# Optimization experiments

Measured on AMD Instinct MI355X. Metric: run time of the kernel, lower is better.

## Reference

```python
import jax, jax.numpy as jnp
import numpy as np

B, S, I = 64, 64, 512      # batch, seq_len, input_size (encoder hidden)
C = 512                    # context_size (attention dim)
H = 1024                   # decoder hidden (must equal 2*deep_out_size per source)
D = 512                    # deep_out_size
KY = 32000                 # target vocab
M = 512                    # target embedding dim (Ey rows)


def setup_inputs() -> dict:
    key = jax.random.key(0)
    ks = jax.random.split(key, 16)
    sc = 0.05  # small init to keep tanh/softmax in sane range
    return {
        "input_seq": jax.random.normal(ks[0], (B, S, I), jnp.float32),
        "Ey_t": jax.random.normal(ks[1], (KY, M), jnp.float32) * sc,   # Ey.transpose(0,1)
        "W":  jax.random.normal(ks[2], (H, C), jnp.float32) * sc,
        "U":  jax.random.normal(ks[3], (I, C), jnp.float32) * sc,
        "b":  jax.random.normal(ks[4], (C,), jnp.float32) * sc,
        "v":  jax.random.normal(ks[5], (C,), jnp.float32) * sc,
        "W_ih": jax.random.normal(ks[6], (3 * H, C), jnp.float32) * sc,
        "W_hh": jax.random.normal(ks[7], (3 * H, H), jnp.float32) * sc,
        "b_ih": jax.random.normal(ks[8], (3 * H,), jnp.float32) * sc,
        "b_hh": jax.random.normal(ks[9], (3 * H,), jnp.float32) * sc,
        "U_o": jax.random.normal(ks[10], (H, H), jnp.float32) * sc,   # (2*D, hidden) with H==2*D
        "V_o": jax.random.normal(ks[11], (M, H), jnp.float32) * sc,
        "C_o": jax.random.normal(ks[12], (I, H), jnp.float32) * sc,
        "W_o": jax.random.normal(ks[13], (D, KY), jnp.float32) * sc,
    }


def reference(input_seq, Ey_t, W, U, b, v, W_ih, W_hh, b_ih, b_hh, U_o, V_o, C_o, W_o):
    Bn, Sn, In = input_seq.shape
    Hn = W.shape[0]
    Ky = W_o.shape[1]

    # Precompute U_h once, as in source: (B, S, C)
    U_h = jnp.einsum('bsi,ic->bsc', input_seq, U)

    def gru_cell(x, h):
        # torch.nn.GRUCell semantics, gate order r, z, n
        gi = x @ W_ih.T + b_ih
        gh = h @ W_hh.T + b_hh
        i_r, i_z, i_n = jnp.split(gi, 3, axis=-1)
        h_r, h_z, h_n = jnp.split(gh, 3, axis=-1)
        r = jax.nn.sigmoid(i_r + h_r)
        z = jax.nn.sigmoid(i_z + h_z)
        n = jnp.tanh(i_n + r * h_n)
        return (1.0 - z) * n + z * h

    def step(carry, _):
        s, y = carry
        # Additive (Bahdanau) attention over full encoder sequence
        W_s = s @ W                                       # (B, C)
        e = jnp.tanh(W_s[:, None, :] + U_h + b) @ v       # (B, S)
        alpha = jax.nn.softmax(e, axis=1)                 # softmax over seq dim
        ctx = jnp.einsum('bsi,bs->bi', input_seq, alpha)  # (B, I)
        s_new = gru_cell(ctx, s)                          # (B, H)
        # Deep-output with maxout (pool_size=2)
        t = s_new @ U_o + (y @ Ey_t) @ V_o + ctx @ C_o    # (B, 2*D)
        t = t.reshape(Bn, -1, 2).max(axis=-1)             # (B, D)
        prob = jax.nn.softmax(t @ W_o, axis=-1)           # (B, Ky)
        return (s_new, prob), prob

    s0 = jnp.zeros((Bn, Hn), input_seq.dtype)
    y0 = jnp.zeros((Bn, Ky), input_seq.dtype)
    _, probs = jax.lax.scan(step, (s0, y0), None, length=Sn)
    return probs  # (S, B, Ky)
```

## Files before the change

kernel.cpp:

```cpp
#include <hip/hip_runtime.h>
#include <cstdint>
#include <cstddef>

typedef __bf16 bf16;
typedef __bf16 bf16x8 __attribute__((ext_vector_type(8)));
typedef float f32x4 __attribute__((ext_vector_type(4)));

#define MFMA16(a, b, c) __builtin_amdgcn_mfma_f32_16x16x32_bf16((a), (b), (c), 0, 0, 0)

__device__ __forceinline__ float fast_tanh(float x) {
  x = fminf(fmaxf(x, -15.f), 15.f);
  float e = __expf(2.f * x);
  return (e - 1.f) / (e + 1.f);
}
__device__ __forceinline__ float fast_sigmoid(float x) {
  return 1.f / (1.f + __expf(-x));
}


__global__ void cast_split_kernel(const float* __restrict__ src,
                                  bf16* __restrict__ hi, bf16* __restrict__ lo, int n) {
  int i = blockIdx.x * 256 + threadIdx.x;
  if (i < n) {
    float x = src[i];
    bf16 h = (bf16)x;
    hi[i] = h;
    lo[i] = (bf16)(x - (float)h);
  }
}

__global__ void tc_kernel(const float* __restrict__ src, bf16* __restrict__ hi,
                          bf16* __restrict__ lo, int R, int C) {
  __shared__ float tile[32][33];
  int c0 = blockIdx.x * 32, r0 = blockIdx.y * 32;
  int tx = threadIdx.x & 31, ty = threadIdx.x >> 5;
  for (int i = ty; i < 32; i += 8)
    tile[i][tx] = src[(size_t)(r0 + i) * C + c0 + tx];
  __syncthreads();
  for (int i = ty; i < 32; i += 8) {
    float x = tile[tx][i];
    bf16 h = (bf16)x;
    size_t idx = (size_t)(c0 + i) * R + r0 + tx;
    hi[idx] = h;
    if (lo) lo[idx] = (bf16)(x - (float)h);
  }
}


template <int ATOMIC>
__device__ __forceinline__ void gemm_body(const bf16* __restrict__ A, int lda,
                                          const bf16* __restrict__ BT, int ldb,
                                          float* __restrict__ C, int ldc,
                                          int mb, int nb, int k0, int kSteps) {
  int lane = threadIdx.x & 63, wave = threadIdx.x >> 6;
  int mrow = mb * 64 + wave * 16 + (lane & 15);
  int qk = (lane >> 4) * 8;
  const bf16* ap = A + (size_t)mrow * lda + k0 + qk;
  int ncol = nb * 64 + (lane & 15);
  const bf16* bp[4];
#pragma unroll
  for (int j = 0; j < 4; ++j) bp[j] = BT + (size_t)(ncol + 16 * j) * ldb + k0 + qk;
  f32x4 acc[4];
#pragma unroll
  for (int j = 0; j < 4; ++j) acc[j] = {0.f, 0.f, 0.f, 0.f};
  for (int s = 0; s < kSteps; ++s) {
    bf16x8 a = *(const bf16x8*)ap; ap += 32;
#pragma unroll
    for (int j = 0; j < 4; ++j) {
      bf16x8 b = *(const bf16x8*)bp[j]; bp[j] += 32;
      acc[j] = MFMA16(a, b, acc[j]);
    }
  }
  int row = mb * 64 + wave * 16 + (lane >> 4) * 4;
  int col = nb * 64 + (lane & 15);
#pragma unroll
  for (int j = 0; j < 4; ++j)
#pragma unroll
    for (int i = 0; i < 4; ++i) {
      size_t idx = (size_t)(row + i) * ldc + col + j * 16;
      if (ATOMIC) atomicAdd(&C[idx], acc[j][i]); else C[idx] = acc[j][i];
    }
}

__device__ __forceinline__ void gemm_split_body(const bf16* __restrict__ Ahi,
                                                const bf16* __restrict__ Alo, int lda,
                                                const bf16* __restrict__ Bhi,
                                                const bf16* __restrict__ Blo, int ldb,
                                                float* __restrict__ C, int ldc,
                                                int mb, int nb, int kSteps) {
  int lane = threadIdx.x & 63, wave = threadIdx.x >> 6;
  int mrow = mb * 64 + wave * 16 + (lane & 15);
  int qk = (lane >> 4) * 8;
  const bf16* ah = Ahi + (size_t)mrow * lda + qk;
  const bf16* al = Alo + (size_t)mrow * lda + qk;
  int ncol = nb * 64 + (lane & 15);
  const bf16* bh[4]; const bf16* bl[4];
#pragma unroll
  for (int j = 0; j < 4; ++j) {
    bh[j] = Bhi + (size_t)(ncol + 16 * j) * ldb + qk;
    bl[j] = Blo + (size_t)(ncol + 16 * j) * ldb + qk;
  }
  f32x4 acc[4];
#pragma unroll
  for (int j = 0; j < 4; ++j) acc[j] = {0.f, 0.f, 0.f, 0.f};
  for (int s = 0; s < kSteps; ++s) {
    bf16x8 Ah = *(const bf16x8*)ah; ah += 32;
    bf16x8 Al = *(const bf16x8*)al; al += 32;
#pragma unroll
    for (int j = 0; j < 4; ++j) {
      bf16x8 Bh = *(const bf16x8*)bh[j]; bh[j] += 32;
      bf16x8 Bl = *(const bf16x8*)bl[j]; bl[j] += 32;
      acc[j] = MFMA16(Ah, Bh, acc[j]);
      acc[j] = MFMA16(Ah, Bl, acc[j]);
      acc[j] = MFMA16(Al, Bh, acc[j]);
    }
  }
  int row = mb * 64 + wave * 16 + (lane >> 4) * 4;
  int col = nb * 64 + (lane & 15);
#pragma unroll
  for (int j = 0; j < 4; ++j)
#pragma unroll
    for (int i = 0; i < 4; ++i)
      C[(size_t)(row + i) * ldc + col + j * 16] = acc[j][i];
}

__global__ __launch_bounds__(256) void gemm_kernel(const bf16* __restrict__ A, int lda,
                                                   const bf16* __restrict__ BT, int ldb,
                                                   float* __restrict__ C, int ldc,
                                                   int nbN, int kSteps) {
  gemm_body<0>(A, lda, BT, ldb, C, ldc, blockIdx.x / nbN, blockIdx.x % nbN, 0, kSteps);
}

__global__ __launch_bounds__(256) void gemm_split_kernel(const bf16* __restrict__ Ahi,
                                                         const bf16* __restrict__ Alo, int lda,
                                                         const bf16* __restrict__ Bhi,
                                                         const bf16* __restrict__ Blo, int ldb,
                                                         float* __restrict__ C, int ldc,
                                                         int nbN, int kSteps) {
  gemm_split_body(Ahi, Alo, lda, Bhi, Blo, ldb, C, ldc, blockIdx.x / nbN, blockIdx.x % nbN, kSteps);
}


__global__ __launch_bounds__(256) void k1_attn_t1(
    const float* __restrict__ Ws, const float* __restrict__ U_h,
    const float* __restrict__ attnb, const float* __restrict__ vvec,
    const float* __restrict__ inseq,
    bf16* __restrict__ ctx_hi, bf16* __restrict__ ctx_lo,
    const bf16* __restrict__ y_bf, const bf16* __restrict__ EyT,
    float* __restrict__ t1f) {
  int bx = blockIdx.x;
  if (bx < 64) {
    __shared__ float sWs[512];
    __shared__ float sV[512];
    __shared__ float sE[64];
    __shared__ float sAl[64];
    int t = threadIdx.x;
    for (int c = t; c < 512; c += 256) {
      sWs[c] = Ws[bx * 512 + c] + attnb[c];
      sV[c] = vvec[c];
    }
    __syncthreads();
    int j = t >> 2, q = t & 3;
    const float* uh = U_h + ((size_t)(bx * 64 + j)) * 512 + q * 128;
    float part = 0.f;
#pragma unroll 4
    for (int c = 0; c < 128; ++c) {
      int cc = q * 128 + c;
      part += sV[cc] * fast_tanh(sWs[cc] + uh[c]);
    }
    part += __shfl_xor(part, 1);
    part += __shfl_xor(part, 2);
    if (q == 0) sE[j] = part;
    __syncthreads();
    if (t < 64) {
      float x = sE[t];
      float m = x;
      for (int off = 32; off; off >>= 1) m = fmaxf(m, __shfl_xor(m, off));
      float a = __expf(x - m);
      float ssum = a;
      for (int off = 32; off; off >>= 1) ssum += __shfl_xor(ssum, off);
      sAl[t] = a / ssum;
    }
    __syncthreads();
    for (int c = t; c < 512; c += 256) {
      float acc = 0.f;
      const float* ip = inseq + ((size_t)bx * 64) * 512 + c;
#pragma unroll 8
      for (int jj = 0; jj < 64; ++jj) acc += sAl[jj] * ip[(size_t)jj * 512];
      bf16 h = (bf16)acc;
      ctx_hi[bx * 512 + c] = h;
      ctx_lo[bx * 512 + c] = (bf16)(acc - (float)h);
    }
  } else {
    int b2 = bx - 64;
    int nb = b2 & 7;
    int kb = b2 >> 3;
    gemm_body<1>(y_bf, 32000, EyT, 32000, t1f, 512, 0, nb, kb * 1280, 40);
  }
}

__global__ __launch_bounds__(256) void k2_gru(
    const bf16* __restrict__ ctx_hi, const bf16* __restrict__ ctx_lo,
    const bf16* __restrict__ s_hi, const bf16* __restrict__ s_lo,
    const bf16* __restrict__ Wih_hi, const bf16* __restrict__ Wih_lo,
    const bf16* __restrict__ Whh_hi, const bf16* __restrict__ Whh_lo,
    const float* __restrict__ b_ih, const float* __restrict__ b_hh,
    const float* __restrict__ s_cur, float* __restrict__ s_next,
    bf16* __restrict__ sn_hi, bf16* __restrict__ sn_lo) {
  int h0 = blockIdx.x * 16;
  int lane = threadIdx.x & 63, wave = threadIdx.x >> 6;
  int m = wave * 16 + (lane & 15);
  int qk = (lane >> 4) * 8;
  int hl = lane & 15;
  f32x4 gi[3], gh[3];
#pragma unroll
  for (int g = 0; g < 3; ++g) { gi[g] = {0.f, 0.f, 0.f, 0.f}; gh[g] = {0.f, 0.f, 0.f, 0.f}; }
  {
    const bf16* ah = ctx_hi + (size_t)m * 512 + qk;
    const bf16* al = ctx_lo + (size_t)m * 512 + qk;
    const bf16* bh[3]; const bf16* bl[3];
#pragma unroll
    for (int g = 0; g < 3; ++g) {
      size_t r = (size_t)(g * 1024 + h0 + hl) * 512 + qk;
      bh[g] = Wih_hi + r; bl[g] = Wih_lo + r;
    }
    for (int s = 0; s < 16; ++s) {
      bf16x8 Ah = *(const bf16x8*)ah; ah += 32;
      bf16x8 Al = *(const bf16x8*)al; al += 32;
#pragma unroll
      for (int g = 0; g < 3; ++g) {
        bf16x8 Bh = *(const bf16x8*)bh[g]; bh[g] += 32;
        bf16x8 Bl = *(const bf16x8*)bl[g]; bl[g] += 32;
        gi[g] = MFMA16(Ah, Bh, gi[g]);
        gi[g] = MFMA16(Ah, Bl, gi[g]);
        gi[g] = MFMA16(Al, Bh, gi[g]);
      }
    }
  }
  {
    const bf16* ah = s_hi + (size_t)m * 1024 + qk;
    const bf16* al = s_lo + (size_t)m * 1024 + qk;
    const bf16* bh[3]; const bf16* bl[3];
#pragma unroll
    for (int g = 0; g < 3; ++g) {
      size_t r = (size_t)(g * 1024 + h0 + hl) * 1024 + qk;
      bh[g] = Whh_hi + r; bl[g] = Whh_lo + r;
    }
    for (int s = 0; s < 32; ++s) {
      bf16x8 Ah = *(const bf16x8*)ah; ah += 32;
      bf16x8 Al = *(const bf16x8*)al; al += 32;
#pragma unroll
      for (int g = 0; g < 3; ++g) {
        bf16x8 Bh = *(const bf16x8*)bh[g]; bh[g] += 32;
        bf16x8 Bl = *(const bf16x8*)bl[g]; bl[g] += 32;
        gh[g] = MFMA16(Ah, Bh, gh[g]);
        gh[g] = MFMA16(Ah, Bl, gh[g]);
        gh[g] = MFMA16(Al, Bh, gh[g]);
      }
    }
  }
  int hg = h0 + hl;
  float bir = b_ih[hg], biz = b_ih[1024 + hg], bin = b_ih[2048 + hg];
  float bhr = b_hh[hg], bhz = b_hh[1024 + hg], bhn = b_hh[2048 + hg];
  int brow0 = wave * 16 + (lane >> 4) * 4;
#pragma unroll
  for (int i = 0; i < 4; ++i) {
    int b = brow0 + i;
    float r = fast_sigmoid(gi[0][i] + bir + gh[0][i] + bhr);
    float z = fast_sigmoid(gi[1][i] + biz + gh[1][i] + bhz);
    float n = fast_tanh(gi[2][i] + bin + r * (gh[2][i] + bhn));
    float so = s_cur[(size_t)b * 1024 + hg];
    float sn = (1.f - z) * n + z * so;
    s_next[(size_t)b * 1024 + hg] = sn;
    bf16 hh = (bf16)sn;
    sn_hi[(size_t)b * 1024 + hg] = hh;
    sn_lo[(size_t)b * 1024 + hg] = (bf16)(sn - (float)hh);
  }
}

__global__ __launch_bounds__(256) void k3_deepout(
    const bf16* __restrict__ sn_hi, const bf16* __restrict__ sn_lo,
    const float* __restrict__ t1f,
    const bf16* __restrict__ ctx_hi, const bf16* __restrict__ ctx_lo,
    const bf16* __restrict__ UoT_hi, const bf16* __restrict__ UoT_lo,
    const bf16* __restrict__ VoT_hi, const bf16* __restrict__ VoT_lo,
    const bf16* __restrict__ CoT_hi, const bf16* __restrict__ CoT_lo,
    const bf16* __restrict__ WT_hi, const bf16* __restrict__ WT_lo,
    bf16* __restrict__ tm_bf, float* __restrict__ Ws_out) {
  int bx = blockIdx.x;
  int lane = threadIdx.x & 63, wave = threadIdx.x >> 6;
  int qk = (lane >> 4) * 8;
  if (bx < 64) {
    int n0 = bx * 16;
    int m = wave * 16 + (lane & 15);
    int nr = n0 + (lane & 15);
    f32x4 acc = {0.f, 0.f, 0.f, 0.f};
    {
      const bf16* ah = sn_hi + (size_t)m * 1024 + qk;
      const bf16* al = sn_lo + (size_t)m * 1024 + qk;
      const bf16* bh = UoT_hi + (size_t)nr * 1024 + qk;
      const bf16* bl = UoT_lo + (size_t)nr * 1024 + qk;
      for (int s = 0; s < 32; ++s) {
        bf16x8 Ah = *(const bf16x8*)ah; ah += 32;
        bf16x8 Al = *(const bf16x8*)al; al += 32;
        bf16x8 Bh = *(const bf16x8*)bh; bh += 32;
        bf16x8 Bl = *(const bf16x8*)bl; bl += 32;
        acc = MFMA16(Ah, Bh, acc); acc = MFMA16(Ah, Bl, acc); acc = MFMA16(Al, Bh, acc);
      }
    }
    {
      const float* ap = t1f + (size_t)m * 512 + qk;
      const bf16* bh = VoT_hi + (size_t)nr * 512 + qk;
      const bf16* bl = VoT_lo + (size_t)nr * 512 + qk;
      for (int s = 0; s < 16; ++s) {
        f32x4 f0 = *(const f32x4*)ap;
        f32x4 f1 = *(const f32x4*)(ap + 4);
        ap += 32;
        bf16x8 Ah, Al;
#pragma unroll
        for (int i = 0; i < 4; ++i) {
          bf16 h = (bf16)f0[i]; Ah[i] = h; Al[i] = (bf16)(f0[i] - (float)h);
          h = (bf16)f1[i]; Ah[4 + i] = h; Al[4 + i] = (bf16)(f1[i] - (float)h);
        }
        bf16x8 Bh = *(const bf16x8*)bh; bh += 32;
        bf16x8 Bl = *(const bf16x8*)bl; bl += 32;
        acc = MFMA16(Ah, Bh, acc); acc = MFMA16(Ah, Bl, acc); acc = MFMA16(Al, Bh, acc);
      }
    }
    {
      const bf16* ah = ctx_hi + (size_t)m * 512 + qk;
      const bf16* al = ctx_lo + (size_t)m * 512 + qk;
      const bf16* bh = CoT_hi + (size_t)nr * 512 + qk;
      const bf16* bl = CoT_lo + (size_t)nr * 512 + qk;
      for (int s = 0; s < 16; ++s) {
        bf16x8 Ah = *(const bf16x8*)ah; ah += 32;
        bf16x8 Al = *(const bf16x8*)al; al += 32;
        bf16x8 Bh = *(const bf16x8*)bh; bh += 32;
        bf16x8 Bl = *(const bf16x8*)bl; bl += 32;
        acc = MFMA16(Ah, Bh, acc); acc = MFMA16(Ah, Bl, acc); acc = MFMA16(Al, Bh, acc);
      }
    }
    int col = lane & 15;
    int row0 = wave * 16 + (lane >> 4) * 4;
#pragma unroll
    for (int i = 0; i < 4; ++i) {
      float vme = acc[i];
      float vot = __shfl_xor(vme, 1);
      float mx = fmaxf(vme, vot);
      if (!(col & 1)) {
        int d = (n0 + col) >> 1;
        tm_bf[(size_t)(row0 + i) * 512 + d] = (bf16)mx;
      }
    }
  } else {
    gemm_split_body(sn_hi, sn_lo, 1024, WT_hi, WT_lo, 1024, Ws_out, 512, 0, bx - 64, 32);
  }
}

__global__ __launch_bounds__(1024) void k5_softmax(
    const float* __restrict__ logits, float* __restrict__ out,
    bf16* __restrict__ y_bf, float* __restrict__ t1f, int step) {
  int b = blockIdx.x, t = threadIdx.x;
  const float* lr = logits + (size_t)b * 32000;
  float x[32];
  float mx = -1e30f;
#pragma unroll
  for (int i = 0; i < 32; ++i) {
    int k = i * 1024 + t;
    if (k < 32000) { float v = lr[k]; x[i] = v; mx = fmaxf(mx, v); }
  }
  __shared__ float red[16];
  int lane = t & 63, wv = t >> 6;
  for (int off = 32; off; off >>= 1) mx = fmaxf(mx, __shfl_xor(mx, off));
  if (lane == 0) red[wv] = mx;
  __syncthreads();
  if (wv == 0) {
    float m2 = (lane < 16) ? red[lane] : -1e30f;
    for (int off = 8; off; off >>= 1) m2 = fmaxf(m2, __shfl_xor(m2, off));
    if (lane == 0) red[0] = m2;
  }
  __syncthreads();
  mx = red[0];
  __syncthreads();
  float sum = 0.f;
#pragma unroll
  for (int i = 0; i < 32; ++i) {
    int k = i * 1024 + t;
    if (k < 32000) { float e = __expf(x[i] - mx); x[i] = e; sum += e; }
  }
  for (int off = 32; off; off >>= 1) sum += __shfl_xor(sum, off);
  if (lane == 0) red[wv] = sum;
  __syncthreads();
  if (wv == 0) {
    float s2 = (lane < 16) ? red[lane] : 0.f;
    for (int off = 8; off; off >>= 1) s2 += __shfl_xor(s2, off);
    if (lane == 0) red[0] = s2;
  }
  __syncthreads();
  float inv = 1.f / red[0];
  float* orow = out + ((size_t)step * 64 + b) * 32000;
  bf16* yrow = y_bf + (size_t)b * 32000;
#pragma unroll
  for (int i = 0; i < 32; ++i) {
    int k = i * 1024 + t;
    if (k < 32000) {
      float p = x[i] * inv;
      orow[k] = p;
      yrow[k] = (bf16)p;
    }
  }
  if (t < 512) t1f[(size_t)b * 512 + t] = 0.f;
}


extern "C" void kernel_launch(void* const* d_in, const int* in_sizes, int n_in,
                              void* d_out, int out_size, void* d_ws, size_t ws_size,
                              hipStream_t stream) {
  const float* input_seq = (const float*)d_in[0];
  const float* Ey_t = (const float*)d_in[1];
  const float* W = (const float*)d_in[2];
  const float* U = (const float*)d_in[3];
  const float* attnb = (const float*)d_in[4];
  const float* vvec = (const float*)d_in[5];
  const float* W_ih = (const float*)d_in[6];
  const float* W_hh = (const float*)d_in[7];
  const float* b_ih = (const float*)d_in[8];
  const float* b_hh = (const float*)d_in[9];
  const float* U_o = (const float*)d_in[10];
  const float* V_o = (const float*)d_in[11];
  const float* C_o = (const float*)d_in[12];
  const float* W_o = (const float*)d_in[13];
  float* out = (float*)d_out;

  char* p = (char*)d_ws;
  auto alloc = [&](size_t bytes) -> char* {
    char* r = p;
    p += (bytes + 255) & ~(size_t)255;
    return r;
  };
  float* sbuf0 = (float*)alloc(64 * 1024 * 4);
  bf16* shi0 = (bf16*)alloc(64 * 1024 * 2);
  bf16* slo0 = (bf16*)alloc(64 * 1024 * 2);
  float* Ws = (float*)alloc(64 * 512 * 4);
  float* t1f = (float*)alloc(64 * 512 * 4);
  bf16* y_bf = (bf16*)alloc((size_t)64 * 32000 * 2);
  size_t zeroBytes = (size_t)(p - (char*)d_ws);
  float* sbuf1 = (float*)alloc(64 * 1024 * 4);
  bf16* shi1 = (bf16*)alloc(64 * 1024 * 2);
  bf16* slo1 = (bf16*)alloc(64 * 1024 * 2);
  bf16* ctx_hi = (bf16*)alloc(64 * 512 * 2);
  bf16* ctx_lo = (bf16*)alloc(64 * 512 * 2);
  bf16* tm_bf = (bf16*)alloc(64 * 512 * 2);
  float* logits = (float*)alloc((size_t)64 * 32000 * 4);
  float* U_h = (float*)alloc((size_t)4096 * 512 * 4);
  bf16* in_hi = (bf16*)alloc((size_t)4096 * 512 * 2);
  bf16* in_lo = (bf16*)alloc((size_t)4096 * 512 * 2);
  bf16* UT_hi = (bf16*)alloc(512 * 512 * 2);
  bf16* UT_lo = (bf16*)alloc(512 * 512 * 2);
  bf16* EyT = (bf16*)alloc((size_t)512 * 32000 * 2);
  bf16* WoT = (bf16*)alloc((size_t)32000 * 512 * 2);
  bf16* UoT_hi = (bf16*)alloc((size_t)1024 * 1024 * 2);
  bf16* UoT_lo = (bf16*)alloc((size_t)1024 * 1024 * 2);
  bf16* VoT_hi = (bf16*)alloc((size_t)1024 * 512 * 2);
  bf16* VoT_lo = (bf16*)alloc((size_t)1024 * 512 * 2);
  bf16* CoT_hi = (bf16*)alloc((size_t)1024 * 512 * 2);
  bf16* CoT_lo = (bf16*)alloc((size_t)1024 * 512 * 2);
  bf16* WT_hi = (bf16*)alloc((size_t)512 * 1024 * 2);
  bf16* WT_lo = (bf16*)alloc((size_t)512 * 1024 * 2);
  bf16* Wih_hi = (bf16*)alloc((size_t)3072 * 512 * 2);
  bf16* Wih_lo = (bf16*)alloc((size_t)3072 * 512 * 2);
  bf16* Whh_hi = (bf16*)alloc((size_t)3072 * 1024 * 2);
  bf16* Whh_lo = (bf16*)alloc((size_t)3072 * 1024 * 2);

  hipMemsetAsync(d_ws, 0, zeroBytes, stream);

  cast_split_kernel<<<(4096 * 512) / 256, 256, 0, stream>>>(input_seq, in_hi, in_lo, 4096 * 512);
  cast_split_kernel<<<(3072 * 512) / 256, 256, 0, stream>>>(W_ih, Wih_hi, Wih_lo, 3072 * 512);
  cast_split_kernel<<<(3072 * 1024) / 256, 256, 0, stream>>>(W_hh, Whh_hi, Whh_lo, 3072 * 1024);
  tc_kernel<<<dim3(512 / 32, 512 / 32), 256, 0, stream>>>(U, UT_hi, UT_lo, 512, 512);
  tc_kernel<<<dim3(512 / 32, 32000 / 32), 256, 0, stream>>>(Ey_t, EyT, nullptr, 32000, 512);
  tc_kernel<<<dim3(32000 / 32, 512 / 32), 256, 0, stream>>>(W_o, WoT, nullptr, 512, 32000);
  tc_kernel<<<dim3(1024 / 32, 1024 / 32), 256, 0, stream>>>(U_o, UoT_hi, UoT_lo, 1024, 1024);
  tc_kernel<<<dim3(1024 / 32, 512 / 32), 256, 0, stream>>>(V_o, VoT_hi, VoT_lo, 512, 1024);
  tc_kernel<<<dim3(1024 / 32, 512 / 32), 256, 0, stream>>>(C_o, CoT_hi, CoT_lo, 512, 1024);
  tc_kernel<<<dim3(512 / 32, 1024 / 32), 256, 0, stream>>>(W, WT_hi, WT_lo, 1024, 512);
  gemm_split_kernel<<<64 * 8, 256, 0, stream>>>(in_hi, in_lo, 512, UT_hi, UT_lo, 512,
                                                U_h, 512, 8, 16);

  float* sb[2] = {sbuf0, sbuf1};
  bf16* sh[2] = {shi0, shi1};
  bf16* sl[2] = {slo0, slo1};

  for (int t = 0; t < 64; ++t) {
    int cur = t & 1;
    k1_attn_t1<<<264, 256, 0, stream>>>(Ws, U_h, attnb, vvec, input_seq,
                                        ctx_hi, ctx_lo, y_bf, EyT, t1f);
    k2_gru<<<64, 256, 0, stream>>>(ctx_hi, ctx_lo, sh[cur], sl[cur],
                                   Wih_hi, Wih_lo, Whh_hi, Whh_lo, b_ih, b_hh,
                                   sb[cur], sb[cur ^ 1], sh[cur ^ 1], sl[cur ^ 1]);
    k3_deepout<<<72, 256, 0, stream>>>(sh[cur ^ 1], sl[cur ^ 1], t1f, ctx_hi, ctx_lo,
                                       UoT_hi, UoT_lo, VoT_hi, VoT_lo, CoT_hi, CoT_lo,
                                       WT_hi, WT_lo, tm_bf, Ws);
    gemm_kernel<<<500, 256, 0, stream>>>(tm_bf, 512, WoT, 512, logits, 32000, 500, 16);
    k5_softmax<<<64, 1024, 0, stream>>>(logits, out, y_bf, t1f, t);
  }
  (void)in_sizes; (void)n_in; (void)out_size; (void)ws_size;
}
```

Before: 10.25 ms.

## Fuse per-step decoder kernels into one cooperative persistent mega-kernel

Replaces the five kernel launches per time step (64 steps) with a single cooperative kernel of 256 blocks that uses grid.sync between phases. Softmax is restructured so the output GEMM epilogue computes exp and per-tile partial sums, with normalization deferred to the next step's attention phase. The unnormalized exp values are fed directly into the Ey GEMM and rescaled by 1/Z. The GRU and deep-out GEMMs are also split across K into two wave groups with an LDS reduction. The aim is to remove launch overhead and the separate logits/softmax passes, at the cost of grid-wide barriers and fewer active blocks per phase. Softmax no longer subtracts the row max before exp, which risks overflow for larger logits.

Result: slower. 16.67 ms (+62.7%).

```diff
diff --git a/kernel.cpp b/kernel.cpp
--- a/kernel.cpp
+++ b/kernel.cpp
@@ -1,6 +1,9 @@
 #include <hip/hip_runtime.h>
+#include <hip/hip_cooperative_groups.h>
 #include <cstdint>
 #include <cstddef>
+
+namespace cg = cooperative_groups;
 
 typedef __bf16 bf16;
 typedef __bf16 bf16x8 __attribute__((ext_vector_type(8)));
@@ -46,42 +49,6 @@
   }
 }
 
-
-template <int ATOMIC>
-__device__ __forceinline__ void gemm_body(const bf16* __restrict__ A, int lda,
-                                          const bf16* __restrict__ BT, int ldb,
-                                          float* __restrict__ C, int ldc,
-                                          int mb, int nb, int k0, int kSteps) {
-  int lane = threadIdx.x & 63, wave = threadIdx.x >> 6;
-  int mrow = mb * 64 + wave * 16 + (lane & 15);
-  int qk = (lane >> 4) * 8;
-  const bf16* ap = A + (size_t)mrow * lda + k0 + qk;
-  int ncol = nb * 64 + (lane & 15);
-  const bf16* bp[4];
-#pragma unroll
-  for (int j = 0; j < 4; ++j) bp[j] = BT + (size_t)(ncol + 16 * j) * ldb + k0 + qk;
-  f32x4 acc[4];
-#pragma unroll
-  for (int j = 0; j < 4; ++j) acc[j] = {0.f, 0.f, 0.f, 0.f};
-  for (int s = 0; s < kSteps; ++s) {
-    bf16x8 a = *(const bf16x8*)ap; ap += 32;
-#pragma unroll
-    for (int j = 0; j < 4; ++j) {
-      bf16x8 b = *(const bf16x8*)bp[j]; bp[j] += 32;
-      acc[j] = MFMA16(a, b, acc[j]);
-    }
-  }
-  int row = mb * 64 + wave * 16 + (lane >> 4) * 4;
-  int col = nb * 64 + (lane & 15);
-#pragma unroll
-  for (int j = 0; j < 4; ++j)
-#pragma unroll
-    for (int i = 0; i < 4; ++i) {
-      size_t idx = (size_t)(row + i) * ldc + col + j * 16;
-      if (ATOMIC) atomicAdd(&C[idx], acc[j][i]); else C[idx] = acc[j][i];
-    }
-}
-
 __device__ __forceinline__ void gemm_split_body(const bf16* __restrict__ Ahi,
                                                 const bf16* __restrict__ Alo, int lda,
                                                 const bf16* __restrict__ Bhi,
@@ -103,6 +70,7 @@
   f32x4 acc[4];
 #pragma unroll
   for (int j = 0; j < 4; ++j) acc[j] = {0.f, 0.f, 0.f, 0.f};
+#pragma unroll 2
   for (int s = 0; s < kSteps; ++s) {
     bf16x8 Ah = *(const bf16x8*)ah; ah += 32;
     bf16x8 Al = *(const bf16x8*)al; al += 32;
@@ -124,13 +92,6 @@
       C[(size_t)(row + i) * ldc + col + j * 16] = acc[j][i];
 }
 
-__global__ __launch_bounds__(256) void gemm_kernel(const bf16* __restrict__ A, int lda,
-                                                   const bf16* __restrict__ BT, int ldb,
-                                                   float* __restrict__ C, int ldc,
-                                                   int nbN, int kSteps) {
-  gemm_body<0>(A, lda, BT, ldb, C, ldc, blockIdx.x / nbN, blockIdx.x % nbN, 0, kSteps);
-}
-
 __global__ __launch_bounds__(256) void gemm_split_kernel(const bf16* __restrict__ Ahi,
                                                          const bf16* __restrict__ Alo, int lda,
                                                          const bf16* __restrict__ Bhi,
@@ -141,275 +102,422 @@
 }
 
 
-__global__ __launch_bounds__(256) void k1_attn_t1(
-    const float* __restrict__ Ws, const float* __restrict__ U_h,
-    const float* __restrict__ attnb, const float* __restrict__ vvec,
-    const float* __restrict__ inseq,
-    bf16* __restrict__ ctx_hi, bf16* __restrict__ ctx_lo,
-    const bf16* __restrict__ y_bf, const bf16* __restrict__ EyT,
-    float* __restrict__ t1f) {
-  int bx = blockIdx.x;
-  if (bx < 64) {
-    __shared__ float sWs[512];
-    __shared__ float sV[512];
-    __shared__ float sE[64];
-    __shared__ float sAl[64];
-    int t = threadIdx.x;
-    for (int c = t; c < 512; c += 256) {
-      sWs[c] = Ws[bx * 512 + c] + attnb[c];
-      sV[c] = vvec[c];
+struct MegaArgs {
+  const float* U_h; const float* attnb; const float* vvec; const float* inseq;
+  float* Ws;
+  bf16* ctx_hi; bf16* ctx_lo;
+  bf16* Ebf; const bf16* EyT; float* t1f;
+  float* Ef; float* Zpart; float* invZ; float* out;
+  float* sbuf0; float* sbuf1; bf16* shi0; bf16* slo0; bf16* shi1; bf16* slo1;
+  const bf16* Wih_hi; const bf16* Wih_lo; const bf16* Whh_hi; const bf16* Whh_lo;
+  const float* b_ih; const float* b_hh;
+  const bf16* UoT_hi; const bf16* UoT_lo; const bf16* VoT_hi; const bf16* VoT_lo;
+  const bf16* CoT_hi; const bf16* CoT_lo; const bf16* WT_hi; const bf16* WT_lo;
+  const bf16* WoT; bf16* tm_bf;
+};
+
+__global__ __launch_bounds__(512) void mega_kernel(MegaArgs a) {
+  cg::grid_group grid = cg::this_grid();
+  __shared__ __align__(16) float smem[6400];
+  int bx = blockIdx.x, tid = threadIdx.x;
+  int lane = tid & 63, wave = tid >> 6;
+  int half = tid >> 8, vt = tid & 255;
+
+  for (int t = 0; t < 64; ++t) {
+    const float* s_cur = (t & 1) ? a.sbuf1 : a.sbuf0;
+    float* s_nxt = (t & 1) ? a.sbuf0 : a.sbuf1;
+    const bf16* shc = (t & 1) ? a.shi1 : a.shi0;
+    const bf16* slc = (t & 1) ? a.slo1 : a.slo0;
+    bf16* shn = (t & 1) ? a.shi0 : a.shi1;
+    bf16* sln = (t & 1) ? a.slo0 : a.slo1;
+
+    if (bx < 32) {
+      int b = bx * 2 + half;
+      float* sWs = smem;
+      float* sV = smem + 1024;
+      float* sE = smem + 2048;
+      float* sAl = smem + 2176;
+      float* w4 = smem + 2304;
+      float part0 = 0.f;
+      if (t > 0)
+        for (int nb = vt; nb < 500; nb += 256) part0 += a.Zpart[nb * 64 + b];
+#pragma unroll
+      for (int off = 32; off; off >>= 1) part0 += __shfl_xor(part0, off);
+      if ((vt & 63) == 0) w4[half * 4 + (vt >> 6)] = part0;
+      for (int c = vt; c < 512; c += 256) {
+        sWs[half * 512 + c] = a.Ws[b * 512 + c] + a.attnb[c];
+        sV[half * 512 + c] = a.vvec[c];
+      }
+      __syncthreads();
+      float iz = (t == 0) ? 0.f
+                          : 1.f / (w4[half * 4] + w4[half * 4 + 1] + w4[half * 4 + 2] + w4[half * 4 + 3]);
+      if (vt == 0) a.invZ[b] = iz;
+      int j = vt >> 2, q = vt & 3;
+      const float* uh = a.U_h + ((size_t)(b * 64 + j)) * 512 + q * 128;
+      const float* Wsb = sWs + half * 512;
+      const float* Vb = sV + half * 512;
+      float part = 0.f;
+#pragma unroll 4
+      for (int c = 0; c < 128; ++c) {
+        int cc = q * 128 + c;
+        part += Vb[cc] * fast_tanh(Wsb[cc] + uh[c]);
+      }
+      part += __shfl_xor(part, 1);
+      part += __shfl_xor(part, 2);
+      if (q == 0) sE[half * 64 + j] = part;
+      __syncthreads();
+      if (vt < 64) {
+        float x = sE[half * 64 + vt];
+        float m = x;
+        for (int off = 32; off; off >>= 1) m = fmaxf(m, __shfl_xor(m, off));
+        float aa = __expf(x - m);
+        float ss = aa;
+        for (int off = 32; off; off >>= 1) ss += __shfl_xor(ss, off);
+        sAl[half * 64 + vt] = aa / ss;
+      }
+      __syncthreads();
+      for (int c = vt; c < 512; c += 256) {
+        float acc = 0.f;
+        const float* ip = a.inseq + ((size_t)b * 64) * 512 + c;
+#pragma unroll 8
+        for (int jj = 0; jj < 64; ++jj) acc += sAl[half * 64 + jj] * ip[(size_t)jj * 512];
+        bf16 hh = (bf16)acc;
+        a.ctx_hi[b * 512 + c] = hh;
+        a.ctx_lo[b * 512 + c] = (bf16)(acc - (float)hh);
+      }
+      if (t > 0) {
+        const f32x4* er = (const f32x4*)(a.Ef + (size_t)b * 32000);
+        f32x4* orow = (f32x4*)(a.out + ((size_t)(t - 1) * 64 + b) * 32000);
+        for (int v = vt; v < 8000; v += 256) {
+          f32x4 e = er[v];
+          f32x4 o = {e[0] * iz, e[1] * iz, e[2] * iz, e[3] * iz};
+          orow[v] = o;
+        }
+      }
+    } else {
+      int vb = bx * 2 + half;
+      if (vb < 464) {
+        int b2 = vb - 64, nb = b2 & 7, kb = b2 >> 3;
+        int l = vt & 63, wv = vt >> 6;
+        int mrow = wv * 16 + (l & 15);
+        int qk = (l >> 4) * 8;
+        const bf16* ap = a.Ebf + (size_t)mrow * 32000 + kb * 640 + qk;
+        int ncol = nb * 64 + (l & 15);
+        const bf16* bp[4];
+#pragma unroll
+        for (int jj = 0; jj < 4; ++jj)
+          bp[jj] = a.EyT + (size_t)(ncol + 16 * jj) * 32000 + kb * 640 + qk;
+        f32x4 acc[4];
+#pragma unroll
+        for (int jj = 0; jj < 4; ++jj) acc[jj] = {0.f, 0.f, 0.f, 0.f};
+#pragma unroll 4
+        for (int s = 0; s < 20; ++s) {
+          bf16x8 av = *(const bf16x8*)ap; ap += 32;
+#pragma unroll
+          for (int jj = 0; jj < 4; ++jj) {
+            bf16x8 bv = *(const bf16x8*)bp[jj]; bp[jj] += 32;
+            acc[jj] = MFMA16(av, bv, acc[jj]);
+          }
+        }
+        int row = wv * 16 + (l >> 4) * 4;
+        int col = nb * 64 + (l & 15);
+#pragma unroll
+        for (int jj = 0; jj < 4; ++jj)
+#pragma unroll
+          for (int i = 0; i < 4; ++i)
+            atomicAdd(&a.t1f[(size_t)(row + i) * 512 + col + jj * 16], acc[jj][i]);
+      }
     }
-    __syncthreads();
-    int j = t >> 2, q = t & 3;
-    const float* uh = U_h + ((size_t)(bx * 64 + j)) * 512 + q * 128;
-    float part = 0.f;
-#pragma unroll 4
-    for (int c = 0; c < 128; ++c) {
-      int cc = q * 128 + c;
-      part += sV[cc] * fast_tanh(sWs[cc] + uh[c]);
+    grid.sync();
+
+    if (bx < 64) {
+      int h0 = bx * 16;
+      int rw = wave & 3, kg = wave >> 2;
+      int m = rw * 16 + (lane & 15);
+      int qk = (lane >> 4) * 8;
+      int hl = lane & 15;
+      f32x4 gi[3], gh[3];
+#pragma unroll
+      for (int g = 0; g < 3; ++g) { gi[g] = {0.f, 0.f, 0.f, 0.f}; gh[g] = {0.f, 0.f, 0.f, 0.f}; }
+      {
+        const bf16* ah = a.ctx_hi + (size_t)m * 512 + kg * 256 + qk;
+        const bf16* al = a.ctx_lo + (size_t)m * 512 + kg * 256 + qk;
+        const bf16* bh[3]; const bf16* bl[3];
+#pragma unroll
+        for (int g = 0; g < 3; ++g) {
+          size_t r = (size_t)(g * 1024 + h0 + hl) * 512 + kg * 256 + qk;
+          bh[g] = a.Wih_hi + r; bl[g] = a.Wih_lo + r;
+        }
+#pragma unroll 4
+        for (int s = 0; s < 8; ++s) {
+          bf16x8 Ah = *(const bf16x8*)ah; ah += 32;
+          bf16x8 Al = *(const bf16x8*)al; al += 32;
+#pragma unroll
+          for (int g = 0; g < 3; ++g) {
+            bf16x8 Bh = *(const bf16x8*)bh[g]; bh[g] += 32;
+            bf16x8 Bl = *(const bf16x8*)bl[g]; bl[g] += 32;
+            gi[g] = MFMA16(Ah, Bh, gi[g]);
+            gi[g] = MFMA16(Ah, Bl, gi[g]);
+            gi[g] = MFMA16(Al, Bh, gi[g]);
+          }
+        }
+      }
+      {
+        const bf16* ah = shc + (size_t)m * 1024 + kg * 512 + qk;
+        const bf16* al = slc + (size_t)m * 1024 + kg * 512 + qk;
+        const bf16* bh[3]; const bf16* bl[3];
+#pragma unroll
+        for (int g = 0; g < 3; ++g) {
+          size_t r = (size_t)(g * 1024 + h0 + hl) * 1024 + kg * 512 + qk;
+          bh[g] = a.Whh_hi + r; bl[g] = a.Whh_lo + r;
+        }
+#pragma unroll 4
+        for (int s = 0; s < 16; ++s) {
+          bf16x8 Ah = *(const bf16x8*)ah; ah += 32;
+          bf16x8 Al = *(const bf16x8*)al; al += 32;
+#pragma unroll
+          for (int g = 0; g < 3; ++g) {
+            bf16x8 Bh = *(const bf16x8*)bh[g]; bh[g] += 32;
+            bf16x8 Bl = *(const bf16x8*)bl[g]; bl[g] += 32;
+            gh[g] = MFMA16(Ah, Bh, gh[g]);
+            gh[g] = MFMA16(Ah, Bl, gh[g]);
+            gh[g] = MFMA16(Al, Bh, gh[g]);
+          }
+        }
+      }
+      float* red = smem;
+      if (kg == 1) {
+        float* d = red + (rw * 64 + lane) * 25;
+#pragma unroll
+        for (int g = 0; g < 3; ++g)
+#pragma unroll
+          for (int i = 0; i < 4; ++i) { d[g * 4 + i] = gi[g][i]; d[12 + g * 4 + i] = gh[g][i]; }
+      }
+      __syncthreads();
+      if (kg == 0) {
+        const float* d = red + (rw * 64 + lane) * 25;
+#pragma unroll
+        for (int g = 0; g < 3; ++g)
+#pragma unroll
+          for (int i = 0; i < 4; ++i) { gi[g][i] += d[g * 4 + i]; gh[g][i] += d[12 + g * 4 + i]; }
+        int hg = h0 + hl;
+        float bir = a.b_ih[hg], biz = a.b_ih[1024 + hg], bin = a.b_ih[2048 + hg];
+        float bhr = a.b_hh[hg], bhz = a.b_hh[1024 + hg], bhn = a.b_hh[2048 + hg];
+        int brow0 = rw * 16 + (lane >> 4) * 4;
+#pragma unroll
+        for (int i = 0; i < 4; ++i) {
+          int b = brow0 + i;
+          float r = fast_sigmoid(gi[0][i] + bir + gh[0][i] + bhr);
+          float z = fast_sigmoid(gi[1][i] + biz + gh[1][i] + bhz);
+          float n = fast_tanh(gi[2][i] + bin + r * (gh[2][i] + bhn));
+          float so = s_cur[(size_t)b * 1024 + hg];
+          float sn = (1.f - z) * n + z * so;
+          s_nxt[(size_t)b * 1024 + hg] = sn;
+          bf16 hh = (bf16)sn;
+          shn[(size_t)b * 1024 + hg] = hh;
+          sln[(size_t)b * 1024 + hg] = (bf16)(sn - (float)hh);
+        }
+      }
     }
-    part += __shfl_xor(part, 1);
-    part += __shfl_xor(part, 2);
-    if (q == 0) sE[j] = part;
-    __syncthreads();
-    if (t < 64) {
-      float x = sE[t];
-      float m = x;
-      for (int off = 32; off; off >>= 1) m = fmaxf(m, __shfl_xor(m, off));
-      float a = __expf(x - m);
-      float ssum = a;
-      for (int off = 32; off; off >>= 1) ssum += __shfl_xor(ssum, off);
-      sAl[t] = a / ssum;
-    }
-    __syncthreads();
-    for (int c = t; c < 512; c += 256) {
-      float acc = 0.f;
-      const float* ip = inseq + ((size_t)bx * 64) * 512 + c;
-#pragma unroll 8
-      for (int jj = 0; jj < 64; ++jj) acc += sAl[jj] * ip[(size_t)jj * 512];
-      bf16 h = (bf16)acc;
-      ctx_hi[bx * 512 + c] = h;
-      ctx_lo[bx * 512 + c] = (bf16)(acc - (float)h);
-    }
-  } else {
-    int b2 = bx - 64;
-    int nb = b2 & 7;
-    int kb = b2 >> 3;
-    gemm_body<1>(y_bf, 32000, EyT, 32000, t1f, 512, 0, nb, kb * 1280, 40);
-  }
-}
-
-__global__ __launch_bounds__(256) void k2_gru(
-    const bf16* __restrict__ ctx_hi, const bf16* __restrict__ ctx_lo,
-    const bf16* __restrict__ s_hi, const bf16* __restrict__ s_lo,
-    const bf16* __restrict__ Wih_hi, const bf16* __restrict__ Wih_lo,
-    const bf16* __restrict__ Whh_hi, const bf16* __restrict__ Whh_lo,
-    const float* __restrict__ b_ih, const float* __restrict__ b_hh,
-    const float* __restrict__ s_cur, float* __restrict__ s_next,
-    bf16* __restrict__ sn_hi, bf16* __restrict__ sn_lo) {
-  int h0 = blockIdx.x * 16;
-  int lane = threadIdx.x & 63, wave = threadIdx.x >> 6;
-  int m = wave * 16 + (lane & 15);
-  int qk = (lane >> 4) * 8;
-  int hl = lane & 15;
-  f32x4 gi[3], gh[3];
-#pragma unroll
-  for (int g = 0; g < 3; ++g) { gi[g] = {0.f, 0.f, 0.f, 0.f}; gh[g] = {0.f, 0.f, 0.f, 0.f}; }
-  {
-    const bf16* ah = ctx_hi + (size_t)m * 512 + qk;
-    const bf16* al = ctx_lo + (size_t)m * 512 + qk;
-    const bf16* bh[3]; const bf16* bl[3];
-#pragma unroll
-    for (int g = 0; g < 3; ++g) {
-      size_t r = (size_t)(g * 1024 + h0 + hl) * 512 + qk;
-      bh[g] = Wih_hi + r; bl[g] = Wih_lo + r;
-    }
-    for (int s = 0; s < 16; ++s) {
-      bf16x8 Ah = *(const bf16x8*)ah; ah += 32;
-      bf16x8 Al = *(const bf16x8*)al; al += 32;
-#pragma unroll
-      for (int g = 0; g < 3; ++g) {
-        bf16x8 Bh = *(const bf16x8*)bh[g]; bh[g] += 32;
-        bf16x8 Bl = *(const bf16x8*)bl[g]; bl[g] += 32;
-        gi[g] = MFMA16(Ah, Bh, gi[g]);
-        gi[g] = MFMA16(Ah, Bl, gi[g]);
-        gi[g] = MFMA16(Al, Bh, gi[g]);
-      }
-    }
-  }
-  {
-    const bf16* ah = s_hi + (size_t)m * 1024 + qk;
-    const bf16* al = s_lo + (size_t)m * 1024 + qk;
-    const bf16* bh[3]; const bf16* bl[3];
-#pragma unroll
-    for (int g = 0; g < 3; ++g) {
-      size_t r = (size_t)(g * 1024 + h0 + hl) * 1024 + qk;
-      bh[g] = Whh_hi + r; bl[g] = Whh_lo + r;
-    }
-    for (int s = 0; s < 32; ++s) {
-      bf16x8 Ah = *(const bf16x8*)ah; ah += 32;
-      bf16x8 Al = *(const bf16x8*)al; al += 32;
-#pragma unroll
-      for (int g = 0; g < 3; ++g) {
-        bf16x8 Bh = *(const bf16x8*)bh[g]; bh[g] += 32;
-        bf16x8 Bl = *(const bf16x8*)bl[g]; bl[g] += 32;
-        gh[g] = MFMA16(Ah, Bh, gh[g]);
-        gh[g] = MFMA16(Ah, Bl, gh[g]);
-        gh[g] = MFMA16(Al, Bh, gh[g]);
-      }
-    }
-  }
-  int hg = h0 + hl;
-  float bir = b_ih[hg], biz = b_ih[1024 + hg], bin = b_ih[2048 + hg];
-  float bhr = b_hh[hg], bhz = b_hh[1024 + hg], bhn = b_hh[2048 + hg];
-  int brow0 = wave * 16 + (lane >> 4) * 4;
-#pragma unroll
-  for (int i = 0; i < 4; ++i) {
-    int b = brow0 + i;
-    float r = fast_sigmoid(gi[0][i] + bir + gh[0][i] + bhr);
-    float z = fast_sigmoid(gi[1][i] + biz + gh[1][i] + bhz);
-    float n = fast_tanh(gi[2][i] + bin + r * (gh[2][i] + bhn));
-    float so = s_cur[(size_t)b * 1024 + hg];
-    float sn = (1.f - z) * n + z * so;
-    s_next[(size_t)b * 1024 + hg] = sn;
-    bf16 hh = (bf16)sn;
-    sn_hi[(size_t)b * 1024 + hg] = hh;
-    sn_lo[(size_t)b * 1024 + hg] = (bf16)(sn - (float)hh);
-  }
-}
-
-__global__ __launch_bounds__(256) void k3_deepout(
-    const bf16* __restrict__ sn_hi, const bf16* __restrict__ sn_lo,
-    const float* __restrict__ t1f,
-    const bf16* __restrict__ ctx_hi, const bf16* __restrict__ ctx_lo,
-    const bf16* __restrict__ UoT_hi, const bf16* __restrict__ UoT_lo,
-    const bf16* __restrict__ VoT_hi, const bf16* __restrict__ VoT_lo,
-    const bf16* __restrict__ CoT_hi, const bf16* __restrict__ CoT_lo,
-    const bf16* __restrict__ WT_hi, const bf16* __restrict__ WT_lo,
-    bf16* __restrict__ tm_bf, float* __restrict__ Ws_out) {
-  int bx = blockIdx.x;
-  int lane = threadIdx.x & 63, wave = threadIdx.x >> 6;
-  int qk = (lane >> 4) * 8;
-  if (bx < 64) {
-    int n0 = bx * 16;
-    int m = wave * 16 + (lane & 15);
-    int nr = n0 + (lane & 15);
-    f32x4 acc = {0.f, 0.f, 0.f, 0.f};
-    {
-      const bf16* ah = sn_hi + (size_t)m * 1024 + qk;
-      const bf16* al = sn_lo + (size_t)m * 1024 + qk;
-      const bf16* bh = UoT_hi + (size_t)nr * 1024 + qk;
-      const bf16* bl = UoT_lo + (size_t)nr * 1024 + qk;
-      for (int s = 0; s < 32; ++s) {
-        bf16x8 Ah = *(const bf16x8*)ah; ah += 32;
-        bf16x8 Al = *(const bf16x8*)al; al += 32;
-        bf16x8 Bh = *(const bf16x8*)bh; bh += 32;
-        bf16x8 Bl = *(const bf16x8*)bl; bl += 32;
-        acc = MFMA16(Ah, Bh, acc); acc = MFMA16(Ah, Bl, acc); acc = MFMA16(Al, Bh, acc);
-      }
-    }
-    {
-      const float* ap = t1f + (size_t)m * 512 + qk;
-      const bf16* bh = VoT_hi + (size_t)nr * 512 + qk;
-      const bf16* bl = VoT_lo + (size_t)nr * 512 + qk;
-      for (int s = 0; s < 16; ++s) {
-        f32x4 f0 = *(const f32x4*)ap;
-        f32x4 f1 = *(const f32x4*)(ap + 4);
-        ap += 32;
-        bf16x8 Ah, Al;
+    grid.sync();
+
+    if (bx < 64) {
+      int n0 = bx * 16;
+      int rw = wave & 3, kg = wave >> 2;
+      int m = rw * 16 + (lane & 15);
+      int nr = n0 + (lane & 15);
+      int qk = (lane >> 4) * 8;
+      f32x4 acc = {0.f, 0.f, 0.f, 0.f};
+      if (kg == 0) {
+        const bf16* ah = shn + (size_t)m * 1024 + qk;
+        const bf16* al = sln + (size_t)m * 1024 + qk;
+        const bf16* bh = a.UoT_hi + (size_t)nr * 1024 + qk;
+        const bf16* bl = a.UoT_lo + (size_t)nr * 1024 + qk;
+#pragma unroll 4
+        for (int s = 0; s < 32; ++s) {
+          bf16x8 Ah = *(const bf16x8*)ah; ah += 32;
+          bf16x8 Al = *(const bf16x8*)al; al += 32;
+          bf16x8 Bh = *(const bf16x8*)bh; bh += 32;
+          bf16x8 Bl = *(const bf16x8*)bl; bl += 32;
+          acc = MFMA16(Ah, Bh, acc); acc = MFMA16(Ah, Bl, acc); acc = MFMA16(Al, Bh, acc);
+        }
+      } else {
+        float iz = a.invZ[m];
+        const float* ap = a.t1f + (size_t)m * 512 + qk;
+        const bf16* bh = a.VoT_hi + (size_t)nr * 512 + qk;
+        const bf16* bl = a.VoT_lo + (size_t)nr * 512 + qk;
+#pragma unroll 4
+        for (int s = 0; s < 16; ++s) {
+          f32x4 f0 = *(const f32x4*)ap;
+          f32x4 f1 = *(const f32x4*)(ap + 4);
+          ap += 32;
+          bf16x8 Ah, Al;
+#pragma unroll
+          for (int i = 0; i < 4; ++i) {
+            float x = f0[i] * iz; bf16 hv = (bf16)x; Ah[i] = hv; Al[i] = (bf16)(x - (float)hv);
+            x = f1[i] * iz; hv = (bf16)x; Ah[4 + i] = hv; Al[4 + i] = (bf16)(x - (float)hv);
+          }
+          bf16x8 Bh = *(const bf16x8*)bh; bh += 32;
+          bf16x8 Bl = *(const bf16x8*)bl; bl += 32;
+          acc = MFMA16(Ah, Bh, acc); acc = MFMA16(Ah, Bl, acc); acc = MFMA16(Al, Bh, acc);
+        }
+        const bf16* ah = a.ctx_hi + (size_t)m * 512 + qk;
+        const bf16* al2 = a.ctx_lo + (size_t)m * 512 + qk;
+        const bf16* bh2 = a.CoT_hi + (size_t)nr * 512 + qk;
+        const bf16* bl2 = a.CoT_lo + (size_t)nr * 512 + qk;
+#pragma unroll 4
+        for (int s = 0; s < 16; ++s) {
+          bf16x8 Ah = *(const bf16x8*)ah; ah += 32;
+          bf16x8 Al = *(const bf16x8*)al2; al2 += 32;
+          bf16x8 Bh = *(const bf16x8*)bh2; bh2 += 32;
+          bf16x8 Bl = *(const bf16x8*)bl2; bl2 += 32;
+          acc = MFMA16(Ah, Bh, acc); acc = MFMA16(Ah, Bl, acc); acc = MFMA16(Al, Bh, acc);
+        }
+      }
+      f32x4* redD = (f32x4*)smem;
+      if (kg == 1) redD[rw * 64 + lane] = acc;
+      __syncthreads();
+      if (kg == 0) {
+        f32x4 o = redD[rw * 64 + lane];
+        acc = acc + o;
+        int col = lane & 15;
+        int row0 = rw * 16 + (lane >> 4) * 4;
 #pragma unroll
         for (int i = 0; i < 4; ++i) {
-          bf16 h = (bf16)f0[i]; Ah[i] = h; Al[i] = (bf16)(f0[i] - (float)h);
-          h = (bf16)f1[i]; Ah[4 + i] = h; Al[4 + i] = (bf16)(f1[i] - (float)h);
-        }
-        bf16x8 Bh = *(const bf16x8*)bh; bh += 32;
-        bf16x8 Bl = *(const bf16x8*)bl; bl += 32;
-        acc = MFMA16(Ah, Bh, acc); acc = MFMA16(Ah, Bl, acc); acc = MFMA16(Al, Bh, acc);
-      }
-    }
-    {
-      const bf16* ah = ctx_hi + (size_t)m * 512 + qk;
-      const bf16* al = ctx_lo + (size_t)m * 512 + qk;
-      const bf16* bh = CoT_hi + (size_t)nr * 512 + qk;
-      const bf16* bl = CoT_lo + (size_t)nr * 512 + qk;
+          float vme = acc[i];
+          float vot = __shfl_xor(vme, 1);
+          float mx = fmaxf(vme, vot);
+          if (!(col & 1)) {
+            int d = (n0 + col) >> 1;
+            a.tm_bf[(size_t)(row0 + i) * 512 + d] = (bf16)mx;
+          }
+        }
+      }
+    } else if (bx < 72) {
+      int nb = bx - 64;
+      int rw = wave & 3, kg = wave >> 2;
+      int m = rw * 16 + (lane & 15);
+      int ncol = nb * 64 + (lane & 15);
+      int qk = (lane >> 4) * 8;
+      const bf16* ah = shn + (size_t)m * 1024 + kg * 512 + qk;
+      const bf16* al = sln + (size_t)m * 1024 + kg * 512 + qk;
+      const bf16* bh[4]; const bf16* bl[4];
+#pragma unroll
+      for (int jj = 0; jj < 4; ++jj) {
+        size_t r = (size_t)(ncol + 16 * jj) * 1024 + kg * 512 + qk;
+        bh[jj] = a.WT_hi + r; bl[jj] = a.WT_lo + r;
+      }
+      f32x4 acc[4];
+#pragma unroll
+      for (int jj = 0; jj < 4; ++jj) acc[jj] = {0.f, 0.f, 0.f, 0.f};
+#pragma unroll 2
       for (int s = 0; s < 16; ++s) {
         bf16x8 Ah = *(const bf16x8*)ah; ah += 32;
         bf16x8 Al = *(const bf16x8*)al; al += 32;
-        bf16x8 Bh = *(const bf16x8*)bh; bh += 32;
-        bf16x8 Bl = *(const bf16x8*)bl; bl += 32;
-        acc = MFMA16(Ah, Bh, acc); acc = MFMA16(Ah, Bl, acc); acc = MFMA16(Al, Bh, acc);
+#pragma unroll
+        for (int jj = 0; jj < 4; ++jj) {
+          bf16x8 Bh = *(const bf16x8*)bh[jj]; bh[jj] += 32;
+          bf16x8 Bl = *(const bf16x8*)bl[jj]; bl[jj] += 32;
+          acc[jj] = MFMA16(Ah, Bh, acc[jj]);
+          acc[jj] = MFMA16(Ah, Bl, acc[jj]);
+          acc[jj] = MFMA16(Al, Bh, acc[jj]);
+        }
+      }
+      f32x4* redW = (f32x4*)smem;
+      if (kg == 1) {
+#pragma unroll
+        for (int jj = 0; jj < 4; ++jj) redW[(rw * 64 + lane) * 5 + jj] = acc[jj];
+      }
+      __syncthreads();
+      if (kg == 0) {
+#pragma unroll
+        for (int jj = 0; jj < 4; ++jj) {
+          f32x4 o = redW[(rw * 64 + lane) * 5 + jj];
+          acc[jj] = acc[jj] + o;
+        }
+        int row = rw * 16 + (lane >> 4) * 4;
+#pragma unroll
+        for (int jj = 0; jj < 4; ++jj)
+#pragma unroll
+          for (int i = 0; i < 4; ++i)
+            a.Ws[(size_t)(row + i) * 512 + nb * 64 + (lane & 15) + jj * 16] = acc[jj][i];
       }
     }
-    int col = lane & 15;
-    int row0 = wave * 16 + (lane >> 4) * 4;
-#pragma unroll
-    for (int i = 0; i < 4; ++i) {
-      float vme = acc[i];
-      float vot = __shfl_xor(vme, 1);
-      float mx = fmaxf(vme, vot);
-      if (!(col & 1)) {
-        int d = (n0 + col) >> 1;
-        tm_bf[(size_t)(row0 + i) * 512 + d] = (bf16)mx;
+    grid.sync();
+
+    {
+      int vb = bx * 2 + half;
+      if (vb < 500) {
+        if (vb < 64) {
+          a.t1f[vb * 512 + vt] = 0.f;
+          a.t1f[vb * 512 + 256 + vt] = 0.f;
+        }
+        int l = vt & 63, wv = vt >> 6;
+        int mrow = wv * 16 + (l & 15);
+        int qk = (l >> 4) * 8;
+        const bf16* ap = a.tm_bf + (size_t)mrow * 512 + qk;
+        int ncol = vb * 64 + (l & 15);
+        const bf16* bp[4];
+#pragma unroll
+        for (int jj = 0; jj < 4; ++jj) bp[jj] = a.WoT + (size_t)(ncol + 16 * jj) * 512 + qk;
+        f32x4 acc[4];
+#pragma unroll
+        for (int jj = 0; jj < 4; ++jj) acc[jj] = {0.f, 0.f, 0.f, 0.f};
+#pragma unroll 4
+        for (int s = 0; s < 16; ++s) {
+          bf16x8 av = *(const bf16x8*)ap; ap += 32;
+#pragma unroll
+          for (int jj = 0; jj < 4; ++jj) {
+            bf16x8 bv = *(const bf16x8*)bp[jj]; bp[jj] += 32;
+            acc[jj] = MFMA16(av, bv, acc[jj]);
+          }
+        }
+        int row0 = wv * 16 + (l >> 4) * 4;
+        int col = vb * 64 + (l & 15);
+        float rs[4] = {0.f, 0.f, 0.f, 0.f};
+#pragma unroll
+        for (int jj = 0; jj < 4; ++jj)
+#pragma unroll
+          for (int i = 0; i < 4; ++i) {
+            float e = __expf(acc[jj][i]);
+            size_t idx = (size_t)(row0 + i) * 32000 + col + jj * 16;
+            a.Ef[idx] = e;
+            a.Ebf[idx] = (bf16)e;
+            rs[i] += e;
+          }
+#pragma unroll
+        for (int i = 0; i < 4; ++i) {
+          float s = rs[i];
+          s += __shfl_xor(s, 1); s += __shfl_xor(s, 2); s += __shfl_xor(s, 4); s += __shfl_xor(s, 8);
+          rs[i] = s;
+        }
+        if ((l & 15) == 0) {
+#pragma unroll
+          for (int i = 0; i < 4; ++i) a.Zpart[vb * 64 + row0 + i] = rs[i];
+        }
       }
     }
-  } else {
-    gemm_split_body(sn_hi, sn_lo, 1024, WT_hi, WT_lo, 1024, Ws_out, 512, 0, bx - 64, 32);
+    grid.sync();
   }
-}
-
-__global__ __launch_bounds__(1024) void k5_softmax(
-    const float* __restrict__ logits, float* __restrict__ out,
-    bf16* __restrict__ y_bf, float* __restrict__ t1f, int step) {
-  int b = blockIdx.x, t = threadIdx.x;
-  const float* lr = logits + (size_t)b * 32000;
-  float x[32];
-  float mx = -1e30f;
-#pragma unroll
-  for (int i = 0; i < 32; ++i) {
-    int k = i * 1024 + t;
-    if (k < 32000) { float v = lr[k]; x[i] = v; mx = fmaxf(mx, v); }
-  }
-  __shared__ float red[16];
-  int lane = t & 63, wv = t >> 6;
-  for (int off = 32; off; off >>= 1) mx = fmaxf(mx, __shfl_xor(mx, off));
-  if (lane == 0) red[wv] = mx;
-  __syncthreads();
-  if (wv == 0) {
-    float m2 = (lane < 16) ? red[lane] : -1e30f;
-    for (int off = 8; off; off >>= 1) m2 = fmaxf(m2, __shfl_xor(m2, off));
-    if (lane == 0) red[0] = m2;
-  }
-  __syncthreads();
-  mx = red[0];
-  __syncthreads();
-  float sum = 0.f;
-#pragma unroll
-  for (int i = 0; i < 32; ++i) {
-    int k = i * 1024 + t;
-    if (k < 32000) { float e = __expf(x[i] - mx); x[i] = e; sum += e; }
-  }
-  for (int off = 32; off; off >>= 1) sum += __shfl_xor(sum, off);
-  if (lane == 0) red[wv] = sum;
-  __syncthreads();
-  if (wv == 0) {
-    float s2 = (lane < 16) ? red[lane] : 0.f;
-    for (int off = 8; off; off >>= 1) s2 += __shfl_xor(s2, off);
-    if (lane == 0) red[0] = s2;
-  }
-  __syncthreads();
-  float inv = 1.f / red[0];
-  float* orow = out + ((size_t)step * 64 + b) * 32000;
-  bf16* yrow = y_bf + (size_t)b * 32000;
-#pragma unroll
-  for (int i = 0; i < 32; ++i) {
-    int k = i * 1024 + t;
-    if (k < 32000) {
-      float p = x[i] * inv;
-      orow[k] = p;
-      yrow[k] = (bf16)p;
+
+  if (bx < 32) {
+    int b = bx * 2 + half;
+    float part = 0.f;
+    for (int nb = vt; nb < 500; nb += 256) part += a.Zpart[nb * 64 + b];
+#pragma unroll
+    for (int off = 32; off; off >>= 1) part += __shfl_xor(part, off);
+    float* w4 = smem;
+    if ((vt & 63) == 0) w4[half * 4 + (vt >> 6)] = part;
+    __syncthreads();
+    float iz = 1.f / (w4[half * 4] + w4[half * 4 + 1] + w4[half * 4 + 2] + w4[half * 4 + 3]);
+    const f32x4* er = (const f32x4*)(a.Ef + (size_t)b * 32000);
+    f32x4* orow = (f32x4*)(a.out + ((size_t)63 * 64 + b) * 32000);
+    for (int v = vt; v < 8000; v += 256) {
+      f32x4 e = er[v];
+      f32x4 o = {e[0] * iz, e[1] * iz, e[2] * iz, e[3] * iz};
+      orow[v] = o;
     }
   }
-  if (t < 512) t1f[(size_t)b * 512 + t] = 0.f;
 }
 
 
@@ -451,7 +559,9 @@
   bf16* ctx_hi = (bf16*)alloc(64 * 512 * 2);
   bf16* ctx_lo = (bf16*)alloc(64 * 512 * 2);
   bf16* tm_bf = (bf16*)alloc(64 * 512 * 2);
-  float* logits = (float*)alloc((size_t)64 * 32000 * 4);
+  float* Ef = (float*)alloc((size_t)64 * 32000 * 4);
+  float* Zpart = (float*)alloc((size_t)500 * 64 * 4);
+  float* invZ = (float*)alloc(64 * 4);
   float* U_h = (float*)alloc((size_t)4096 * 512 * 4);
   bf16* in_hi = (bf16*)alloc((size_t)4096 * 512 * 2);
   bf16* in_lo = (bf16*)alloc((size_t)4096 * 512 * 2);
@@ -487,22 +597,22 @@
   gemm_split_kernel<<<64 * 8, 256, 0, stream>>>(in_hi, in_lo, 512, UT_hi, UT_lo, 512,
                                                 U_h, 512, 8, 16);
 
-  float* sb[2] = {sbuf0, sbuf1};
-  bf16* sh[2] = {shi0, shi1};
-  bf16* sl[2] = {slo0, slo1};
-
-  for (int t = 0; t < 64; ++t) {
-    int cur = t & 1;
-    k1_attn_t1<<<264, 256, 0, stream>>>(Ws, U_h, attnb, vvec, input_seq,
-                                        ctx_hi, ctx_lo, y_bf, EyT, t1f);
-    k2_gru<<<64, 256, 0, stream>>>(ctx_hi, ctx_lo, sh[cur], sl[cur],
-                                   Wih_hi, Wih_lo, Whh_hi, Whh_lo, b_ih, b_hh,
-                                   sb[cur], sb[cur ^ 1], sh[cur ^ 1], sl[cur ^ 1]);
-    k3_deepout<<<72, 256, 0, stream>>>(sh[cur ^ 1], sl[cur ^ 1], t1f, ctx_hi, ctx_lo,
-                                       UoT_hi, UoT_lo, VoT_hi, VoT_lo, CoT_hi, CoT_lo,
-                                       WT_hi, WT_lo, tm_bf, Ws);
-    gemm_kernel<<<500, 256, 0, stream>>>(tm_bf, 512, WoT, 512, logits, 32000, 500, 16);
-    k5_softmax<<<64, 1024, 0, stream>>>(logits, out, y_bf, t1f, t);
-  }
+  MegaArgs ma;
+  ma.U_h = U_h; ma.attnb = attnb; ma.vvec = vvec; ma.inseq = input_seq;
+  ma.Ws = Ws;
+  ma.ctx_hi = ctx_hi; ma.ctx_lo = ctx_lo;
+  ma.Ebf = y_bf; ma.EyT = EyT; ma.t1f = t1f;
+  ma.Ef = Ef; ma.Zpart = Zpart; ma.invZ = invZ; ma.out = out;
+  ma.sbuf0 = sbuf0; ma.sbuf1 = sbuf1;
+  ma.shi0 = shi0; ma.slo0 = slo0; ma.shi1 = shi1; ma.slo1 = slo1;
+  ma.Wih_hi = Wih_hi; ma.Wih_lo = Wih_lo; ma.Whh_hi = Whh_hi; ma.Whh_lo = Whh_lo;
+  ma.b_ih = b_ih; ma.b_hh = b_hh;
+  ma.UoT_hi = UoT_hi; ma.UoT_lo = UoT_lo; ma.VoT_hi = VoT_hi; ma.VoT_lo = VoT_lo;
+  ma.CoT_hi = CoT_hi; ma.CoT_lo = CoT_lo; ma.WT_hi = WT_hi; ma.WT_lo = WT_lo;
+  ma.WoT = WoT; ma.tm_bf = tm_bf;
+
+  void* kargs[] = {&ma};
+  hipLaunchCooperativeKernel((const void*)mega_kernel, dim3(256), dim3(512), kargs, 0, stream);
+
   (void)in_sizes; (void)n_in; (void)out_size; (void)ws_size;
 }
```
